# Kernel tuning notes

Hardware: AMD Instinct MI355X
Metric: run time of the kernel (lower is better)

Reference implementation:

```python
import jax, jax.numpy as jnp
import numpy as np

K = 20
EPS = 1e-5
NEG_SLOPE = 0.2


def knn_idx(x, k):
    # x: (B, C, N) -> idx: (B, N, k) of nearest neighbors by L2 distance
    inner = jnp.einsum('bcn,bcm->bnm', x, x)          # (B, N, N)
    xx = jnp.sum(x * x, axis=1)                        # (B, N)
    # negative squared distance: larger = closer
    neg_dist = 2.0 * inner - xx[:, :, None] - xx[:, None, :]
    _, idx = jax.lax.top_k(neg_dist, k)                # (B, N, k)
    return idx


def edge_feature(x, k):
    # x: (B, C, N) -> (B, 2C, N, k): concat(neighbor - x, x)
    idx = knn_idx(x, k)                                # (B, N, k)
    # neighbors[b,c,n,j] = x[b, c, idx[b,n,j]]
    nbr = jnp.take_along_axis(x[:, :, None, :], idx[:, None, :, :], axis=3)  # (B,C,N,k)
    xc = x[:, :, :, None]
    return jnp.concatenate([nbr - xc, jnp.broadcast_to(xc, nbr.shape)], axis=1)


def conv_bn_lrelu(h, W, gamma, beta):
    # 1x1 conv: h (B, Cin, N, k), W (Cout, Cin)
    h = jnp.einsum('oc,bcnk->bonk', W, h)
    # training-mode BatchNorm2d over (B, N, k) per channel
    mean = jnp.mean(h, axis=(0, 2, 3), keepdims=True)
    var = jnp.var(h, axis=(0, 2, 3), keepdims=True)
    h = (h - mean) * jax.lax.rsqrt(var + EPS)
    h = h * gamma[None, :, None, None] + beta[None, :, None, None]
    return jnp.where(h >= 0, h, NEG_SLOPE * h)


def setup_inputs() -> dict:
    key = jax.random.key(0)
    ks = jax.random.split(key, 3)
    B, C, N = 16, 3, 4096
    x = jax.random.normal(ks[0], (B, C, N), dtype=jnp.float32)
    W0 = jax.random.normal(ks[1], (64, 2 * C), dtype=jnp.float32) * (1.0 / np.sqrt(2 * C))
    W1 = jax.random.normal(ks[2], (64, 64), dtype=jnp.float32) * (1.0 / np.sqrt(64))
    g0 = jnp.ones((64,), jnp.float32); b0 = jnp.zeros((64,), jnp.float32)
    g1 = jnp.ones((64,), jnp.float32); b1 = jnp.zeros((64,), jnp.float32)
    return {"x": x, "W0": W0, "g0": g0, "b0": b0, "W1": W1, "g1": g1, "b1": b1}


def reference(x, W0, g0, b0, W1, g1, b1):
    h = edge_feature(x, K)                 # (B, 2C, N, k)
    h = conv_bn_lrelu(h, W0, g0, b0)       # (B, 64, N, k)
    h = conv_bn_lrelu(h, W1, g1, b1)       # (B, 64, N, k)
    return jnp.max(h, axis=-1)             # (B, 64, N)
```

## Files before the change

### kernel.cpp

```cpp
#include <hip/hip_runtime.h>
#include <cfloat>

#define NEG_SLOPE 0.2f
#define BN_EPS 1e-5f
#define EDGES 1310720
#define INV_M (1.0f / 1310720.0f)

typedef short v8s __attribute__((ext_vector_type(8)));
typedef float v4f __attribute__((ext_vector_type(4)));

__device__ __forceinline__ unsigned short f2bf(float f) {
  unsigned b = __float_as_uint(f);
  b += 0x7fffu + ((b >> 16) & 1u);
  return (unsigned short)(b >> 16);
}
__device__ __forceinline__ float bf2f(unsigned short s) {
  return __uint_as_float(((unsigned)s) << 16);
}

__device__ __forceinline__ float sqnorm_np(float c0, float c1, float c2) {
#pragma clang fp contract(off)
  return (c0 * c0 + c1 * c1) + c2 * c2;
}
__device__ __forceinline__ float negdist2_np(float c0, float c1, float c2,
                                             float q0, float q1, float q2,
                                             float xxn, float xxm) {
#pragma clang fp contract(off)
  float inner2 = (c0 * q0 + c1 * q1) + c2 * q2;
  return (inner2 - xxn) - xxm;
}

template <int PAT>
__device__ __forceinline__ float swzf(float v) {
  return __uint_as_float((unsigned)__builtin_amdgcn_ds_swizzle((int)__float_as_uint(v), PAT));
}
template <int PAT>
__device__ __forceinline__ int swzi(int v) {
  return __builtin_amdgcn_ds_swizzle(v, PAT);
}
__device__ __forceinline__ float bpermf(int addr, float v) {
  return __uint_as_float((unsigned)__builtin_amdgcn_ds_bpermute(addr, (int)__float_as_uint(v)));
}
__device__ __forceinline__ int bpermi(int addr, int v) {
  return __builtin_amdgcn_ds_bpermute(addr, v);
}
__device__ __forceinline__ int imin2(int a, int b) { return a < b ? a : b; }

__device__ __forceinline__ unsigned orderkey(float f) {
  unsigned u = __float_as_uint(f);
  return ((int)u < 0) ? ~u : (u | 0x80000000u);
}
__device__ __forceinline__ int mbcnt64(unsigned long long m) {
  return __builtin_amdgcn_mbcnt_hi((unsigned)(m >> 32),
         __builtin_amdgcn_mbcnt_lo((unsigned)m, 0));
}
__device__ __forceinline__ int wsum3(int c) {
  return __popcll(__ballot(c & 1)) + 2 * (int)__popcll(__ballot(c & 2));
}

__device__ __forceinline__ int pick_max(float v0, int i0, int xaddr) {
  float m = fmaxf(v0, swzf<0x041F>(v0));
  m = fmaxf(m, swzf<0x081F>(m));
  m = fmaxf(m, swzf<0x101F>(m));
  m = fmaxf(m, swzf<0x201F>(m));
  m = fmaxf(m, swzf<0x401F>(m));
  float vmax = fmaxf(m, bpermf(xaddr, m));
  unsigned long long mask = __ballot(v0 == vmax);
  if (__popcll(mask) == 1) {
    int L = (int)(__ffsll(mask) - 1);
    return __builtin_amdgcn_readlane(i0, L);
  }
  int t = (v0 == vmax) ? i0 : 0x7fffffff;
  t = imin2(t, swzi<0x041F>(t));
  t = imin2(t, swzi<0x081F>(t));
  t = imin2(t, swzi<0x101F>(t));
  t = imin2(t, swzi<0x201F>(t));
  t = imin2(t, swzi<0x401F>(t));
  t = imin2(t, bpermi(xaddr, t));
  return t;
}

__device__ __forceinline__ void ins3f(float nd, int m,
                                      float& v0, float& v1, float& v2,
                                      int& i0, int& i1, int& i2) {
  bool g0 = nd > v0, g1 = nd > v1, g2 = nd > v2;
  int ni2 = g2 ? (g1 ? i1 : m) : i2;
  int ni1 = g1 ? (g0 ? i0 : m) : i1;
  i0 = g0 ? m : i0;
  float nv1 = __builtin_amdgcn_fmed3f(nd, v0, v1);
  float nv2 = __builtin_amdgcn_fmed3f(nd, v1, v2);
  v0 = fmaxf(v0, nd);
  v1 = nv1; v2 = nv2; i1 = ni1; i2 = ni2;
}

__device__ __forceinline__ void slow_select(float v0, float v1, float v2,
                                            int i0, int i1, int i2,
                                            const float4* xs, float4 q,
                                            int xaddr, int lane, int* outp) {
  unsigned long long rem = 0ull;
  #pragma unroll 1
  for (int r = 0; r < 20; r++) {
    int win = pick_max(v0, i0, xaddr);
    if (lane == r) outp[r] = win;
    bool own = ((win & 63) == lane);
    rem |= own ? (1ull << (win >> 6)) : 0ull;
    v0 = own ? v1 : v0;  i0 = own ? i1 : i0;
    v1 = own ? v2 : v1;  i1 = own ? i2 : i1;
    v2 = own ? -FLT_MAX : v2;  i2 = own ? 0x7fffffff : i2;
    if (own & (v0 == -FLT_MAX)) {
      #pragma unroll 1
      for (int j = 0; j < 64; j++) {
        int m = (j << 6) + lane;
        float4 c = xs[m];
        float nd = negdist2_np(c.x, c.y, c.z, q.x, q.y, q.z, q.w, c.w);
        if ((rem >> j) & 1ull) nd = -FLT_MAX;
        ins3f(nd, m, v0, v1, v2, i0, i1, i2);
      }
    }
  }
}

__global__ __launch_bounds__(1024, 8) void k1_knn(const float* __restrict__ x, int* __restrict__ idxo) {
  __shared__ float4 xs[4096];
  int b   = blockIdx.x >> 5;
  int blk = blockIdx.x & 31;
  const float* xb = x + b * 12288;
  for (int i = threadIdx.x; i < 4096; i += 1024) {
    float a0 = xb[i], a1 = xb[4096 + i], a2 = xb[8192 + i];
    xs[i] = make_float4(2.0f * a0, 2.0f * a1, 2.0f * a2, sqnorm_np(a0, a1, a2));
  }
  __syncthreads();

  int wv = threadIdx.x >> 6;
  int lane = threadIdx.x & 63;
  int wave_id = blk * 16 + wv;
  int xaddr = ((lane ^ 32) << 2);

  #pragma unroll 1
  for (int p = 0; p < 4; p++) {
    int nA = wave_id * 8 + 2 * p;
    int nB = nA + 1;
    float4 rawA = xs[nA];
    float4 rawB = xs[nB];
    float4 qA = make_float4(0.5f * rawA.x, 0.5f * rawA.y, 0.5f * rawA.z, rawA.w);
    float4 qB = make_float4(0.5f * rawB.x, 0.5f * rawB.y, 0.5f * rawB.z, rawB.w);

    float vA0 = -FLT_MAX, vA1 = -FLT_MAX, vA2 = -FLT_MAX;
    float vB0 = -FLT_MAX, vB1 = -FLT_MAX, vB2 = -FLT_MAX;
    int   iA0 = 0x7fffffff, iA1 = 0x7fffffff, iA2 = 0x7fffffff;
    int   iB0 = 0x7fffffff, iB1 = 0x7fffffff, iB2 = 0x7fffffff;
    #pragma unroll 4
    for (int j = 0; j < 64; j++) {
      int m = (j << 6) + lane;
      float4 c = xs[m];
      float ndA = negdist2_np(c.x, c.y, c.z, qA.x, qA.y, qA.z, qA.w, c.w);
      ins3f(ndA, m, vA0, vA1, vA2, iA0, iA1, iA2);
      float ndB = negdist2_np(c.x, c.y, c.z, qB.x, qB.y, qB.z, qB.w, c.w);
      ins3f(ndB, m, vB0, vB1, vB2, iB0, iB1, iB2);
    }

    unsigned kA0 = orderkey(vA0), kA1 = orderkey(vA1), kA2 = orderkey(vA2);
    unsigned kB0 = orderkey(vB0), kB1 = orderkey(vB1), kB2 = orderkey(vB2);
    unsigned loA = 0u, hiA = 0xFFFFFFFFu;
    unsigned loB = 0u, hiB = 0xFFFFFFFFu;
    #pragma unroll 1
    for (int it = 0; it < 32; it++) {
      unsigned midA = loA + ((hiA - loA) >> 1);
      unsigned midB = loB + ((hiB - loB) >> 1);
      int cA = (kA0 > midA) + (kA1 > midA) + (kA2 > midA);
      int cB = (kB0 > midB) + (kB1 > midB) + (kB2 > midB);
      int tA = wsum3(cA);
      int tB = wsum3(cB);
      if (tA <= 19) hiA = midA; else loA = midA + 1;
      if (tB <= 19) hiB = midB; else loB = midB + 1;
    }
    unsigned tA = hiA, tB = hiB;

    int  cgA = (kA0 > tA) + (kA1 > tA) + (kA2 > tA);
    int  ceA = (kA0 == tA) + (kA1 == tA) + (kA2 == tA);
    bool badA = (__ballot(kA2 >= tA) != 0ull) || (wsum3(ceA) != 20 - wsum3(cgA));
    int  cgB = (kB0 > tB) + (kB1 > tB) + (kB2 > tB);
    int  ceB = (kB0 == tB) + (kB1 == tB) + (kB2 == tB);
    bool badB = (__ballot(kB2 >= tB) != 0ull) || (wsum3(ceB) != 20 - wsum3(cgB));

    int baseA = ((b << 12) + nA) * 20;
    int baseB = ((b << 12) + nB) * 20;

    if (!badA) {
      int c = (kA0 >= tA) + (kA1 >= tA) + (kA2 >= tA);
      unsigned long long m1 = __ballot(c >= 1);
      unsigned long long m2 = __ballot(c >= 2);
      unsigned long long m3 = __ballot(c >= 3);
      int n1 = (int)__popcll(m1), n2 = (int)__popcll(m2);
      if (c >= 1) idxo[baseA + mbcnt64(m1)] = iA0;
      if (c >= 2) idxo[baseA + n1 + mbcnt64(m2)] = iA1;
      if (c >= 3) idxo[baseA + n1 + n2 + mbcnt64(m3)] = iA2;
    } else {
      slow_select(vA0, vA1, vA2, iA0, iA1, iA2, xs, qA, xaddr, lane, idxo + baseA);
    }
    if (!badB) {
      int c = (kB0 >= tB) + (kB1 >= tB) + (kB2 >= tB);
      unsigned long long m1 = __ballot(c >= 1);
      unsigned long long m2 = __ballot(c >= 2);
      unsigned long long m3 = __ballot(c >= 3);
      int n1 = (int)__popcll(m1), n2 = (int)__popcll(m2);
      if (c >= 1) idxo[baseB + mbcnt64(m1)] = iB0;
      if (c >= 2) idxo[baseB + n1 + mbcnt64(m2)] = iB1;
      if (c >= 3) idxo[baseB + n1 + n2 + mbcnt64(m3)] = iB2;
    } else {
      slow_select(vB0, vB1, vB2, iB0, iB1, iB2, xs, qB, xaddr, lane, idxo + baseB);
    }
  }
}

__global__ __launch_bounds__(256) void k2_moments(const float* __restrict__ x,
                                                  const int* __restrict__ idxi,
                                                  float* __restrict__ stat) {
  int P = blockIdx.x * 256 + threadIdx.x;
  int b = P >> 12, n = P & 4095;
  const float* xb = x + b * 12288;
  float xn0 = xb[n], xn1 = xb[4096 + n], xn2 = xb[8192 + n];
  const int* ip = idxi + P * 20;
  float Sd0 = 0.f, Sd1 = 0.f, Sd2 = 0.f;
  float S00 = 0.f, S01 = 0.f, S02 = 0.f, S11 = 0.f, S12 = 0.f, S22 = 0.f;
  #pragma unroll 4
  for (int j = 0; j < 20; j++) {
    int m = ip[j];
    float d0 = xb[m] - xn0, d1 = xb[4096 + m] - xn1, d2 = xb[8192 + m] - xn2;
    Sd0 += d0; Sd1 += d1; Sd2 += d2;
    S00 = fmaf(d0, d0, S00); S01 = fmaf(d0, d1, S01); S02 = fmaf(d0, d2, S02);
    S11 = fmaf(d1, d1, S11); S12 = fmaf(d1, d2, S12); S22 = fmaf(d2, d2, S22);
  }
  float acc[27];
  acc[0] = Sd0; acc[1] = Sd1; acc[2] = Sd2;
  acc[3] = 20.f * xn0; acc[4] = 20.f * xn1; acc[5] = 20.f * xn2;
  acc[6] = S00;  acc[7] = S01;  acc[8] = S02;
  acc[9] = Sd0 * xn0;  acc[10] = Sd0 * xn1; acc[11] = Sd0 * xn2;
  acc[12] = S11; acc[13] = S12;
  acc[14] = Sd1 * xn0; acc[15] = Sd1 * xn1; acc[16] = Sd1 * xn2;
  acc[17] = S22;
  acc[18] = Sd2 * xn0; acc[19] = Sd2 * xn1; acc[20] = Sd2 * xn2;
  acc[21] = 20.f * xn0 * xn0; acc[22] = 20.f * xn0 * xn1; acc[23] = 20.f * xn0 * xn2;
  acc[24] = 20.f * xn1 * xn1; acc[25] = 20.f * xn1 * xn2;
  acc[26] = 20.f * xn2 * xn2;
  #pragma unroll
  for (int i = 0; i < 27; i++) {
    float s = acc[i];
    for (int off = 32; off > 0; off >>= 1) s += __shfl_down(s, off);
    acc[i] = s;
  }
  __shared__ float red[4][27];
  int w = threadIdx.x >> 6, lane = threadIdx.x & 63;
  if (lane == 0) {
    #pragma unroll
    for (int i = 0; i < 27; i++) red[w][i] = acc[i];
  }
  __syncthreads();
  if (threadIdx.x < 27) {
    float s = red[0][threadIdx.x] + red[1][threadIdx.x] + red[2][threadIdx.x] + red[3][threadIdx.x];
    atomicAdd(&stat[threadIdx.x], s);
  }
}

__global__ __launch_bounds__(256) void k0_uv(const float* __restrict__ x, const float* __restrict__ W0,
                                             const float* __restrict__ stat,
                                             const float* __restrict__ g0v, const float* __restrict__ b0v,
                                             unsigned short* __restrict__ u, unsigned short* __restrict__ v) {
  int gid = blockIdx.x * 256 + threadIdx.x;
  int p = gid >> 6;
  int c = gid & 63;
  int b = p >> 12, n = p & 4095;

  float w[6];
  #pragma unroll
  for (int i = 0; i < 6; i++) w[i] = W0[c * 6 + i];
  float mean = 0.f;
  #pragma unroll
  for (int i = 0; i < 6; i++) mean += w[i] * stat[i];
  mean *= INV_M;
  float e2 = 0.f;
  int pp = 6;
  #pragma unroll
  for (int i = 0; i < 6; i++) {
    #pragma unroll
    for (int j = i; j < 6; j++) {
      float f = w[i] * w[j] * stat[pp]; pp++;
      e2 += (i == j) ? f : 2.f * f;
    }
  }
  e2 *= INV_M;
  float var = e2 - mean * mean;
  float a = g0v[c] * rsqrtf(var + BN_EPS);
  float bb = b0v[c] - mean * a;

  const float* xb = x + b * 12288;
  float x0 = xb[n], x1 = xb[4096 + n], x2 = xb[8192 + n];
  float uu = a * (w[0] * x0 + w[1] * x1 + w[2] * x2);
  float vv = a * ((w[3] - w[0]) * x0 + (w[4] - w[1]) * x1 + (w[5] - w[2]) * x2) + bb;
  u[gid] = f2bf(uu);
  v[gid] = f2bf(vv);
}

__global__ __launch_bounds__(256, 4) void k4_mfma(const unsigned short* __restrict__ u,
                                                  const unsigned short* __restrict__ v,
                                                  const int* __restrict__ idxi,
                                                  const float* __restrict__ W1,
                                                  float* __restrict__ psum,
                                                  unsigned short* __restrict__ maxb,
                                                  unsigned short* __restrict__ minb) {
  int lane = threadIdx.x & 63;
  int wv = threadIdx.x >> 6;
  int g = blockIdx.x * 4 + wv;
  int G = g * 16;
  int bbase = (G >> 12) << 12;
  int row16 = lane & 15;
  int quad = lane >> 4;

  v8s Bf[4][2];
  #pragma unroll
  for (int t = 0; t < 4; t++) {
    const float* wrow = W1 + (16 * t + row16) * 64 + quad * 8;
    #pragma unroll
    for (int kh = 0; kh < 2; kh++) {
      #pragma unroll
      for (int i = 0; i < 8; i++) Bf[t][kh][i] = (short)f2bf(wrow[kh * 32 + i]);
    }
  }
  const v8s* vrow = (const v8s*)(v + (G + row16) * 64);
  v8s vv0 = vrow[quad], vv1 = vrow[quad + 4];
  float v0f[8], v1f[8];
  #pragma unroll
  for (int i = 0; i < 8; i++) {
    v0f[i] = bf2f((unsigned short)vv0[i]);
    v1f[i] = bf2f((unsigned short)vv1[i]);
  }

  const int* ip = idxi + (G + row16) * 20;

  float mx[4][4], mn[4][4], s2a[4], sq2a[4];
  #pragma unroll
  for (int t = 0; t < 4; t++) {
    #pragma unroll
    for (int i = 0; i < 4; i++) { mx[t][i] = -FLT_MAX; mn[t][i] = FLT_MAX; }
    s2a[t] = 0.f; sq2a[t] = 0.f;
  }

  int m_next = ip[0];
  #pragma unroll 1
  for (int j = 0; j < 20; j++) {
    int m = bbase + m_next;
    if (j < 19) m_next = ip[j + 1];
    const v8s* urow = (const v8s*)(u + m * 64);
    v8s u0 = urow[quad], u1 = urow[quad + 4];
    v8s a0, a1f;
    #pragma unroll
    for (int i = 0; i < 8; i++) {
      float h = bf2f((unsigned short)u0[i]) + v0f[i];
      h = fmaxf(h, 0.2f * h);
      a0[i] = (short)f2bf(h);
      float h2 = bf2f((unsigned short)u1[i]) + v1f[i];
      h2 = fmaxf(h2, 0.2f * h2);
      a1f[i] = (short)f2bf(h2);
    }
    #pragma unroll
    for (int t = 0; t < 4; t++) {
      v4f c = {0.f, 0.f, 0.f, 0.f};
      c = __builtin_amdgcn_mfma_f32_16x16x32_bf16(a0, Bf[t][0], c, 0, 0, 0);
      c = __builtin_amdgcn_mfma_f32_16x16x32_bf16(a1f, Bf[t][1], c, 0, 0, 0);
      #pragma unroll
      for (int i = 0; i < 4; i++) {
        float cv = c[i];
        mx[t][i] = fmaxf(mx[t][i], cv);
        mn[t][i] = fminf(mn[t][i], cv);
        s2a[t] += cv;
        sq2a[t] = fmaf(cv, cv, sq2a[t]);
      }
    }
  }
  #pragma unroll
  for (int t = 0; t < 4; t++) {
    #pragma unroll
    for (int i = 0; i < 4; i++) {
      int P = G + quad * 4 + i;
      maxb[P * 64 + 16 * t + row16] = f2bf(mx[t][i]);
      minb[P * 64 + 16 * t + row16] = f2bf(mn[t][i]);
    }
  }
  #pragma unroll
  for (int t = 0; t < 4; t++) {
    float s = s2a[t], q = sq2a[t];
    s += __shfl_xor(s, 16); q += __shfl_xor(q, 16);
    s += __shfl_xor(s, 32); q += __shfl_xor(q, 32);
    if (quad == 0) {
      int c = 16 * t + row16;
      psum[c * 4096 + g] = s;
      psum[(64 + c) * 4096 + g] = q;
    }
  }
}

__global__ __launch_bounds__(256) void k4b_red(const float* __restrict__ psum, float* __restrict__ s2) {
  int c = blockIdx.x;
  const float* p = psum + c * 4096;
  float s = 0.f;
  for (int i = threadIdx.x; i < 4096; i += 256) s += p[i];
  for (int off = 32; off > 0; off >>= 1) s += __shfl_down(s, off);
  __shared__ float red[4];
  if ((threadIdx.x & 63) == 0) red[threadIdx.x >> 6] = s;
  __syncthreads();
  if (threadIdx.x == 0) s2[c] = red[0] + red[1] + red[2] + red[3];
}

__global__ __launch_bounds__(256) void k5_out(const unsigned short* __restrict__ maxb,
                                              const unsigned short* __restrict__ minb,
                                              const float* __restrict__ s2, const float* __restrict__ g1,
                                              const float* __restrict__ b1, float* __restrict__ out) {
  __shared__ float T[64][65];
  __shared__ float a2s[64], b2s[64];
  int blk = blockIdx.x;
  int b = blk >> 6;
  int n0 = (blk & 63) << 6;
  int t = threadIdx.x;
  if (t < 64) {
    float mean = s2[t] * INV_M;
    float var = s2[64 + t] * INV_M - mean * mean;
    float a = g1[t] * rsqrtf(var + BN_EPS);
    a2s[t] = a;
    b2s[t] = b1[t] - mean * a;
  }
  __syncthreads();
  #pragma unroll
  for (int i = 0; i < 16; i++) {
    int lin = i * 256 + t;
    int r = lin >> 6;
    int c = lin & 63;
    float a = a2s[c];
    int P = (b << 12) + n0 + r;
    float vfp = bf2f((a >= 0.f) ? maxb[P * 64 + c] : minb[P * 64 + c]);
    float z = a * vfp + b2s[c];
    T[c][r] = z >= 0.f ? z : NEG_SLOPE * z;
  }
  __syncthreads();
  #pragma unroll
  for (int i = 0; i < 16; i++) {
    int lin = i * 256 + t;
    int c = lin >> 6;
    int nn = lin & 63;
    out[(b * 64 + c) * 4096 + n0 + nn] = T[c][nn];
  }
}

extern "C" void kernel_launch(void* const* d_in, const int* in_sizes, int n_in,
                              void* d_out, int out_size, void* d_ws, size_t ws_size,
                              hipStream_t stream) {
  const float* x  = (const float*)d_in[0];
  const float* W0 = (const float*)d_in[1];
  const float* g0 = (const float*)d_in[2];
  const float* b0 = (const float*)d_in[3];
  const float* W1 = (const float*)d_in[4];
  const float* g1 = (const float*)d_in[5];
  const float* b1 = (const float*)d_in[6];
  float* out = (float*)d_out;
  char* ws = (char*)d_ws;

  int*            idx  = (int*)(ws + 0);
  float*          stat = (float*)(ws + 5242880);
  float*          s2   = (float*)(ws + 5242880 + 1024);
  float*          part = (float*)(ws + 5244416);
  unsigned short* u    = (unsigned short*)(ws + 7341568);
  unsigned short* v    = (unsigned short*)(ws + 15730176);
  unsigned short* maxb = (unsigned short*)(ws + 24118784);
  unsigned short* minb = (unsigned short*)(ws + 32507392);

  (void)hipMemsetAsync(stat, 0, 128, stream);
  k1_knn    <<<512, 1024, 0, stream>>>(x, idx);
  k2_moments<<<256, 256, 0, stream>>>(x, idx, stat);
  k0_uv     <<<16384, 256, 0, stream>>>(x, W0, stat, g0, b0, u, v);
  k4_mfma   <<<1024, 256, 0, stream>>>(u, v, idx, W1, part, maxb, minb);
  k4b_red   <<<128, 256, 0, stream>>>(part, s2);
  k5_out    <<<1024, 256, 0, stream>>>(maxb, minb, s2, g1, b1, out);
}
```

Before: 432.8 us.

## Keep top-4 per lane in KNN and precompute BN0 coefficients in a tiny kernel

Measured after the change: 401.9 us. 7.1% less time.

```diff
diff --git a/kernel.cpp b/kernel.cpp
--- a/kernel.cpp
+++ b/kernel.cpp
@@ -54,8 +54,9 @@
   return __builtin_amdgcn_mbcnt_hi((unsigned)(m >> 32),
          __builtin_amdgcn_mbcnt_lo((unsigned)m, 0));
 }
-__device__ __forceinline__ int wsum3(int c) {
-  return __popcll(__ballot(c & 1)) + 2 * (int)__popcll(__ballot(c & 2));
+__device__ __forceinline__ int wsum4(int c) {
+  return (int)__popcll(__ballot(c & 1)) + 2 * (int)__popcll(__ballot(c & 2))
+       + 4 * (int)__popcll(__ballot(c & 4));
 }
 
 __device__ __forceinline__ int pick_max(float v0, int i0, int xaddr) {
@@ -91,6 +92,21 @@
   float nv2 = __builtin_amdgcn_fmed3f(nd, v1, v2);
   v0 = fmaxf(v0, nd);
   v1 = nv1; v2 = nv2; i1 = ni1; i2 = ni2;
+}
+
+__device__ __forceinline__ void ins4f(float nd, int m,
+                                      float& v0, float& v1, float& v2, float& v3,
+                                      int& i0, int& i1, int& i2, int& i3) {
+  bool g0 = nd > v0, g1 = nd > v1, g2 = nd > v2, g3 = nd > v3;
+  int ni3 = g3 ? (g2 ? i2 : m) : i3;
+  int ni2 = g2 ? (g1 ? i1 : m) : i2;
+  int ni1 = g1 ? (g0 ? i0 : m) : i1;
+  i0 = g0 ? m : i0;
+  float nv1 = __builtin_amdgcn_fmed3f(nd, v0, v1);
+  float nv2 = __builtin_amdgcn_fmed3f(nd, v1, v2);
+  float nv3 = __builtin_amdgcn_fmed3f(nd, v2, v3);
+  v0 = fmaxf(v0, nd);
+  v1 = nv1; v2 = nv2; v3 = nv3; i1 = ni1; i2 = ni2; i3 = ni3;
 }
 
 __device__ __forceinline__ void slow_select(float v0, float v1, float v2,
@@ -145,68 +161,72 @@
     float4 qA = make_float4(0.5f * rawA.x, 0.5f * rawA.y, 0.5f * rawA.z, rawA.w);
     float4 qB = make_float4(0.5f * rawB.x, 0.5f * rawB.y, 0.5f * rawB.z, rawB.w);
 
-    float vA0 = -FLT_MAX, vA1 = -FLT_MAX, vA2 = -FLT_MAX;
-    float vB0 = -FLT_MAX, vB1 = -FLT_MAX, vB2 = -FLT_MAX;
-    int   iA0 = 0x7fffffff, iA1 = 0x7fffffff, iA2 = 0x7fffffff;
-    int   iB0 = 0x7fffffff, iB1 = 0x7fffffff, iB2 = 0x7fffffff;
+    float vA0 = -FLT_MAX, vA1 = -FLT_MAX, vA2 = -FLT_MAX, vA3 = -FLT_MAX;
+    float vB0 = -FLT_MAX, vB1 = -FLT_MAX, vB2 = -FLT_MAX, vB3 = -FLT_MAX;
+    int   iA0 = 0x7fffffff, iA1 = 0x7fffffff, iA2 = 0x7fffffff, iA3 = 0x7fffffff;
+    int   iB0 = 0x7fffffff, iB1 = 0x7fffffff, iB2 = 0x7fffffff, iB3 = 0x7fffffff;
     #pragma unroll 4
     for (int j = 0; j < 64; j++) {
       int m = (j << 6) + lane;
       float4 c = xs[m];
       float ndA = negdist2_np(c.x, c.y, c.z, qA.x, qA.y, qA.z, qA.w, c.w);
-      ins3f(ndA, m, vA0, vA1, vA2, iA0, iA1, iA2);
+      ins4f(ndA, m, vA0, vA1, vA2, vA3, iA0, iA1, iA2, iA3);
       float ndB = negdist2_np(c.x, c.y, c.z, qB.x, qB.y, qB.z, qB.w, c.w);
-      ins3f(ndB, m, vB0, vB1, vB2, iB0, iB1, iB2);
-    }
-
-    unsigned kA0 = orderkey(vA0), kA1 = orderkey(vA1), kA2 = orderkey(vA2);
-    unsigned kB0 = orderkey(vB0), kB1 = orderkey(vB1), kB2 = orderkey(vB2);
+      ins4f(ndB, m, vB0, vB1, vB2, vB3, iB0, iB1, iB2, iB3);
+    }
+
+    unsigned kA0 = orderkey(vA0), kA1 = orderkey(vA1), kA2 = orderkey(vA2), kA3 = orderkey(vA3);
+    unsigned kB0 = orderkey(vB0), kB1 = orderkey(vB1), kB2 = orderkey(vB2), kB3 = orderkey(vB3);
     unsigned loA = 0u, hiA = 0xFFFFFFFFu;
     unsigned loB = 0u, hiB = 0xFFFFFFFFu;
     #pragma unroll 1
     for (int it = 0; it < 32; it++) {
       unsigned midA = loA + ((hiA - loA) >> 1);
       unsigned midB = loB + ((hiB - loB) >> 1);
-      int cA = (kA0 > midA) + (kA1 > midA) + (kA2 > midA);
-      int cB = (kB0 > midB) + (kB1 > midB) + (kB2 > midB);
-      int tA = wsum3(cA);
-      int tB = wsum3(cB);
+      int cA = (kA0 > midA) + (kA1 > midA) + (kA2 > midA) + (kA3 > midA);
+      int cB = (kB0 > midB) + (kB1 > midB) + (kB2 > midB) + (kB3 > midB);
+      int tA = wsum4(cA);
+      int tB = wsum4(cB);
       if (tA <= 19) hiA = midA; else loA = midA + 1;
       if (tB <= 19) hiB = midB; else loB = midB + 1;
     }
     unsigned tA = hiA, tB = hiB;
 
-    int  cgA = (kA0 > tA) + (kA1 > tA) + (kA2 > tA);
-    int  ceA = (kA0 == tA) + (kA1 == tA) + (kA2 == tA);
-    bool badA = (__ballot(kA2 >= tA) != 0ull) || (wsum3(ceA) != 20 - wsum3(cgA));
-    int  cgB = (kB0 > tB) + (kB1 > tB) + (kB2 > tB);
-    int  ceB = (kB0 == tB) + (kB1 == tB) + (kB2 == tB);
-    bool badB = (__ballot(kB2 >= tB) != 0ull) || (wsum3(ceB) != 20 - wsum3(cgB));
+    int  cgA = (kA0 > tA) + (kA1 > tA) + (kA2 > tA) + (kA3 > tA);
+    int  ceA = (kA0 == tA) + (kA1 == tA) + (kA2 == tA) + (kA3 == tA);
+    bool badA = (__ballot(kA3 >= tA) != 0ull) || (wsum4(ceA) != 20 - wsum4(cgA));
+    int  cgB = (kB0 > tB) + (kB1 > tB) + (kB2 > tB) + (kB3 > tB);
+    int  ceB = (kB0 == tB) + (kB1 == tB) + (kB2 == tB) + (kB3 == tB);
+    bool badB = (__ballot(kB3 >= tB) != 0ull) || (wsum4(ceB) != 20 - wsum4(cgB));
 
     int baseA = ((b << 12) + nA) * 20;
     int baseB = ((b << 12) + nB) * 20;
 
     if (!badA) {
-      int c = (kA0 >= tA) + (kA1 >= tA) + (kA2 >= tA);
+      int c = (kA0 >= tA) + (kA1 >= tA) + (kA2 >= tA) + (kA3 >= tA);
       unsigned long long m1 = __ballot(c >= 1);
       unsigned long long m2 = __ballot(c >= 2);
       unsigned long long m3 = __ballot(c >= 3);
-      int n1 = (int)__popcll(m1), n2 = (int)__popcll(m2);
+      unsigned long long m4 = __ballot(c >= 4);
+      int n1 = (int)__popcll(m1), n2 = (int)__popcll(m2), n3 = (int)__popcll(m3);
       if (c >= 1) idxo[baseA + mbcnt64(m1)] = iA0;
       if (c >= 2) idxo[baseA + n1 + mbcnt64(m2)] = iA1;
       if (c >= 3) idxo[baseA + n1 + n2 + mbcnt64(m3)] = iA2;
+      if (c >= 4) idxo[baseA + n1 + n2 + n3 + mbcnt64(m4)] = iA3;
     } else {
       slow_select(vA0, vA1, vA2, iA0, iA1, iA2, xs, qA, xaddr, lane, idxo + baseA);
     }
     if (!badB) {
-      int c = (kB0 >= tB) + (kB1 >= tB) + (kB2 >= tB);
+      int c = (kB0 >= tB) + (kB1 >= tB) + (kB2 >= tB) + (kB3 >= tB);
       unsigned long long m1 = __ballot(c >= 1);
       unsigned long long m2 = __ballot(c >= 2);
       unsigned long long m3 = __ballot(c >= 3);
-      int n1 = (int)__popcll(m1), n2 = (int)__popcll(m2);
+      unsigned long long m4 = __ballot(c >= 4);
+      int n1 = (int)__popcll(m1), n2 = (int)__popcll(m2), n3 = (int)__popcll(m3);
       if (c >= 1) idxo[baseB + mbcnt64(m1)] = iB0;
       if (c >= 2) idxo[baseB + n1 + mbcnt64(m2)] = iB1;
       if (c >= 3) idxo[baseB + n1 + n2 + mbcnt64(m3)] = iB2;
+      if (c >= 4) idxo[baseB + n1 + n2 + n3 + mbcnt64(m4)] = iB3;
     } else {
       slow_select(vB0, vB1, vB2, iB0, iB1, iB2, xs, qB, xaddr, lane, idxo + baseB);
     }
@@ -262,9 +282,37 @@
   }
 }
 
+__global__ __launch_bounds__(64) void k3c_coef(const float* __restrict__ W0,
+                                               const float* __restrict__ stat,
+                                               const float* __restrict__ g0v, const float* __restrict__ b0v,
+                                               float* __restrict__ ab) {
+  int c = threadIdx.x;
+  float w[6];
+  #pragma unroll
+  for (int i = 0; i < 6; i++) w[i] = W0[c * 6 + i];
+  float mean = 0.f;
+  #pragma unroll
+  for (int i = 0; i < 6; i++) mean += w[i] * stat[i];
+  mean *= INV_M;
+  float e2 = 0.f;
+  int pp = 6;
+  #pragma unroll
+  for (int i = 0; i < 6; i++) {
+    #pragma unroll
+    for (int j = i; j < 6; j++) {
+      float f = w[i] * w[j] * stat[pp]; pp++;
+      e2 += (i == j) ? f : 2.f * f;
+    }
+  }
+  e2 *= INV_M;
+  float var = e2 - mean * mean;
+  float a = g0v[c] * rsqrtf(var + BN_EPS);
+  ab[c] = a;
+  ab[64 + c] = b0v[c] - mean * a;
+}
+
 __global__ __launch_bounds__(256) void k0_uv(const float* __restrict__ x, const float* __restrict__ W0,
-                                             const float* __restrict__ stat,
-                                             const float* __restrict__ g0v, const float* __restrict__ b0v,
+                                             const float* __restrict__ ab,
                                              unsigned short* __restrict__ u, unsigned short* __restrict__ v) {
   int gid = blockIdx.x * 256 + threadIdx.x;
   int p = gid >> 6;
@@ -274,24 +322,8 @@
   float w[6];
   #pragma unroll
   for (int i = 0; i < 6; i++) w[i] = W0[c * 6 + i];
-  float mean = 0.f;
-  #pragma unroll
-  for (int i = 0; i < 6; i++) mean += w[i] * stat[i];
-  mean *= INV_M;
-  float e2 = 0.f;
-  int pp = 6;
-  #pragma unroll
-  for (int i = 0; i < 6; i++) {
-    #pragma unroll
-    for (int j = i; j < 6; j++) {
-      float f = w[i] * w[j] * stat[pp]; pp++;
-      e2 += (i == j) ? f : 2.f * f;
-    }
-  }
-  e2 *= INV_M;
-  float var = e2 - mean * mean;
-  float a = g0v[c] * rsqrtf(var + BN_EPS);
-  float bb = b0v[c] - mean * a;
+  float a  = ab[c];
+  float bb = ab[64 + c];
 
   const float* xb = x + b * 12288;
   float x0 = xb[n], x1 = xb[4096 + n], x2 = xb[8192 + n];
@@ -465,6 +497,7 @@
 
   int*            idx  = (int*)(ws + 0);
   float*          stat = (float*)(ws + 5242880);
+  float*          ab   = (float*)(ws + 5242880 + 512);
   float*          s2   = (float*)(ws + 5242880 + 1024);
   float*          part = (float*)(ws + 5244416);
   unsigned short* u    = (unsigned short*)(ws + 7341568);
@@ -475,7 +508,8 @@
   (void)hipMemsetAsync(stat, 0, 128, stream);
   k1_knn    <<<512, 1024, 0, stream>>>(x, idx);
   k2_moments<<<256, 256, 0, stream>>>(x, idx, stat);
-  k0_uv     <<<16384, 256, 0, stream>>>(x, W0, stat, g0, b0, u, v);
+  k3c_coef  <<<1, 64, 0, stream>>>(W0, stat, g0, b0, ab);
+  k0_uv     <<<16384, 256, 0, stream>>>(x, W0, ab, u, v);
   k4_mfma   <<<1024, 256, 0, stream>>>(u, v, idx, W1, part, maxb, minb);
   k4b_red   <<<128, 256, 0, stream>>>(part, s2);
   k5_out    <<<1024, 256, 0, stream>>>(maxb, minb, s2, g1, b1, out);
```
